# Performance work log

Measured on AMD Instinct MI355X. Metric: run time of the kernel, lower is better.

## Reference

```python
import jax, jax.numpy as jnp
import numpy as np

N, D_IN, UNITS = 8192, 2048, 2048


def setup_inputs() -> dict:
    key = jax.random.key(0)
    ks = jax.random.split(key, 14)
    s_in = 1.0 / np.sqrt(D_IN)
    s_u = 1.0 / np.sqrt(UNITS)
    return {
        "x": jax.random.normal(ks[0], (N, UNITS), jnp.float32),
        "y": jax.random.normal(ks[1], (N, D_IN), jnp.float32),
        # W* act on y (D_IN -> UNITS), U* act on x (UNITS -> UNITS)
        "Wz": jax.random.normal(ks[2], (D_IN, UNITS), jnp.float32) * s_in,
        "bz": jnp.zeros((UNITS,), jnp.float32),
        "Uz": jax.random.normal(ks[3], (UNITS, UNITS), jnp.float32) * s_u,
        "buz": jax.random.normal(ks[4], (UNITS,), jnp.float32) * 0.05,  # glorot-init bias
        "Wr": jax.random.normal(ks[5], (D_IN, UNITS), jnp.float32) * s_in,
        "br": jnp.zeros((UNITS,), jnp.float32),
        "Ur": jax.random.normal(ks[6], (UNITS, UNITS), jnp.float32) * s_u,
        "bur": jnp.zeros((UNITS,), jnp.float32),
        "Wg": jax.random.normal(ks[7], (D_IN, UNITS), jnp.float32) * s_in,
        "bg": jax.random.normal(ks[8], (UNITS,), jnp.float32) * 0.05,  # glorot-init bias
        "Ug": jax.random.normal(ks[9], (UNITS, UNITS), jnp.float32) * s_u,
        "bug": jnp.zeros((UNITS,), jnp.float32),
    }


def reference(x, y, Wz, bz, Uz, buz, Wr, br, Ur, bur, Wg, bg, Ug, bug):
    # Batch the three y-projections and the two x-projections into single GEMMs.
    Wy = y @ jnp.concatenate([Wz, Wr, Wg], axis=1)          # [N, 3*UNITS]
    Ux = x @ jnp.concatenate([Uz, Ur], axis=1)               # [N, 2*UNITS]
    u = Wz.shape[1]
    z = Wy[:, :u] + bz + Ux[:, :u] + buz                     # NOTE: no sigmoid (faithful to source)
    r = Wy[:, u:2 * u] + br + Ux[:, u:] + bur                # NOTE: no sigmoid (faithful to source)
    h = jnp.tanh(Wy[:, 2 * u:] + bg + (r * x) @ Ug + bug)
    return (1.0 - z) * x + z * h
```

## Files before the change

kernel.cpp:

```cpp
#include <hip/hip_runtime.h>
#include <hip/hip_bf16.h>
#include <cstdint>
#include <cmath>

typedef __bf16 bf16;
typedef __bf16 bf16x8 __attribute__((ext_vector_type(8)));
typedef __bf16 bf16x4 __attribute__((ext_vector_type(4)));
typedef float f32x4 __attribute__((ext_vector_type(4)));

#define NROWS 8192
#define UNITS 2048
#define NT 64
#define NSPLIT 32

__device__ __forceinline__ void gload_lds16(const bf16* g, const bf16* lds) {
  __builtin_amdgcn_global_load_lds(
      (const __attribute__((address_space(1))) uint32_t*)(uintptr_t)g,
      (__attribute__((address_space(3))) uint32_t*)(uint32_t)(uintptr_t)lds,
      16, 0, 0);
}

#define BARR do { asm volatile("" ::: "memory"); __builtin_amdgcn_s_barrier(); \
                  asm volatile("" ::: "memory"); } while (0)
#define WAITV4 asm volatile("s_waitcnt vmcnt(4)" ::: "memory")
#define LGKM8  asm volatile("s_waitcnt lgkmcnt(8)" ::: "memory")
#define LGKM0  asm volatile("s_waitcnt lgkmcnt(0)" ::: "memory")

__global__ void pack_xy_kernel(const float* __restrict__ x, const float* __restrict__ y,
                               bf16* __restrict__ xb, bf16* __restrict__ yb) {
  size_t n4 = (size_t)NROWS * UNITS / 4;
  size_t stride = (size_t)gridDim.x * blockDim.x;
  for (size_t i = (size_t)blockIdx.x * blockDim.x + threadIdx.x; i < n4; i += stride) {
    float4 vx = ((const float4*)x)[i];
    float4 vy = ((const float4*)y)[i];
    bf16x4 ox = {(bf16)vx.x, (bf16)vx.y, (bf16)vx.z, (bf16)vx.w};
    bf16x4 oy = {(bf16)vy.x, (bf16)vy.y, (bf16)vy.z, (bf16)vy.w};
    ((bf16x4*)xb)[i] = ox;
    ((bf16x4*)yb)[i] = oy;
  }
}

__global__ void transpose_cvt6_kernel(const float* __restrict__ Wz, const float* __restrict__ Uz,
                                      const float* __restrict__ Wr, const float* __restrict__ Ur,
                                      const float* __restrict__ Wg, const float* __restrict__ Ug,
                                      bf16* __restrict__ Bzr, bf16* __restrict__ Bgt) {
  __shared__ float t[32][33];
  const float* src;
  bf16* dst;
  int koff;
  switch (blockIdx.z) {
    case 0: src = Wz; dst = Bzr;                         koff = 0;    break;
    case 1: src = Uz; dst = Bzr;                         koff = 2048; break;
    case 2: src = Wr; dst = Bzr + (size_t)2048 * 4096;   koff = 0;    break;
    case 3: src = Ur; dst = Bzr + (size_t)2048 * 4096;   koff = 2048; break;
    case 4: src = Wg; dst = Bgt;                         koff = 0;    break;
    default: src = Ug; dst = Bgt;                        koff = 2048; break;
  }
  int j0 = blockIdx.x * 32, k0 = blockIdx.y * 32;
  int tx = threadIdx.x & 31, ty = threadIdx.x >> 5;
#pragma unroll
  for (int i = 0; i < 32; i += 8)
    t[ty + i][tx] = src[(size_t)(k0 + ty + i) * UNITS + j0 + tx];
  __syncthreads();
#pragma unroll
  for (int i = 0; i < 32; i += 8)
    dst[(size_t)(j0 + ty + i) * 4096 + koff + k0 + tx] = (bf16)t[tx][ty + i];
}

template <int EPI>
__global__ __launch_bounds__(512, 2)
void gemm256(const bf16* __restrict__ A0, const bf16* __restrict__ A1,
             const bf16* __restrict__ Bt,
             const float* __restrict__ bias_a, const float* __restrict__ bias_b,
             const float* __restrict__ bias_c, const float* __restrict__ bias_d,
             const float* __restrict__ xin, bf16* __restrict__ zbuf,
             bf16* __restrict__ rxbuf, float* __restrict__ outbuf) {
  __shared__ bf16 LDS[2][32768];
  const int tid = threadIdx.x;
  const int wv = tid >> 6, lane = tid & 63;
  const int wr = wv >> 2, wc = wv & 3;

  const int nl = (int)gridDim.x >> 3;
  const int xc = (int)blockIdx.x & 7;
  const int l = (int)blockIdx.x >> 3;
  const int bxq = nl >> 4;
  const int by = (xc & 1) * 16 + (l & 15);
  const int bx = (xc >> 1) * bxq + (l >> 4);
  const int brow = by * 256;
  const int bcol = bx * 256;

  const int rr = lane >> 2;
  const int kk_st = ((lane & 3) * 8) ^ ((rr & 6) << 2);
  int offA[2][2], offB[2][2], dstA[2][2], dstB[2][2];
#pragma unroll
  for (int H = 0; H < 2; ++H)
#pragma unroll
    for (int c = 0; c < 2; ++c) {
      int ssA = H * 8 + wv;
      offA[H][c] = (brow + c * 128 + (ssA >> 1) * 16 + rr) * 2048 + (ssA & 1) * 32 + kk_st;
      dstA[H][c] = c * 8192 + ssA * 512;
      int ssB = (wv >> 2) * 8 + H * 4 + (wv & 3);
      offB[H][c] = (bcol + c * 128 + (ssB >> 1) * 16 + rr) * 4096 + (ssB & 1) * 32 + kk_st;
      dstB[H][c] = 16384 + c * 8192 + ssB * 512;
    }

  const int lr = lane & 15;
  const int kread = ((lane >> 4) * 8) ^ ((lr & 6) << 2);
  const int abase = wr * 8192 + lr * 32 + kread;
  const int bbase = 16384 + (wc >> 1) * 8192 + (wc & 1) * 4096 + lr * 32 + kread;

#define ST_A(TI, H, BUF)                                                      \
  if ((TI) < NT) {                                                            \
    const bf16* _s = ((TI) < NSPLIT) ? A0 + (size_t)(TI)*64                   \
                                     : A1 + (size_t)((TI)-NSPLIT) * 64;       \
    gload_lds16(_s + offA[H][0], (BUF) + dstA[H][0]);                         \
    gload_lds16(_s + offA[H][1], (BUF) + dstA[H][1]);                         \
  }
#define ST_B(TI, H, BUF)                                                      \
  if ((TI) < NT) {                                                            \
    const bf16* _s = Bt + (size_t)(TI)*64;                                    \
    gload_lds16(_s + offB[H][0], (BUF) + dstB[H][0]);                         \
    gload_lds16(_s + offB[H][1], (BUF) + dstB[H][1]);                         \
  }
#define RD_B(DST, LP, NB)                                                     \
  _Pragma("unroll") for (int n = 0; n < 2; ++n)                               \
  _Pragma("unroll") for (int kh = 0; kh < 2; ++kh)                            \
      DST[n][kh] = *(const bf16x8*)((LP) + bbase + ((n + 2 * (NB)) * 2 + kh) * 512);
#define RD_A(DST, LP, MB)                                                     \
  _Pragma("unroll") for (int m = 0; m < 4; ++m)                               \
  _Pragma("unroll") for (int kh = 0; kh < 2; ++kh)                            \
      DST[m][kh] = *(const bf16x8*)((LP) + abase + ((m + 4 * (MB)) * 2 + kh) * 512);
#define MFMA_Q(AARR, BARR_, MOFF, NOFF)                                       \
  __builtin_amdgcn_s_setprio(1);                                              \
  _Pragma("unroll") for (int kh = 0; kh < 2; ++kh)                            \
  _Pragma("unroll") for (int m = 0; m < 4; ++m)                               \
  _Pragma("unroll") for (int n = 0; n < 2; ++n)                               \
      acc[m + MOFF][n + NOFF] = __builtin_amdgcn_mfma_f32_16x16x32_bf16(      \
          AARR[m][kh], BARR_[n][kh], acc[m + MOFF][n + NOFF], 0, 0, 0);       \
  __builtin_amdgcn_s_setprio(0);

  f32x4 acc[8][4];
#pragma unroll
  for (int m = 0; m < 8; ++m)
#pragma unroll
    for (int n = 0; n < 4; ++n) {
      f32x4 zz = {0.f, 0.f, 0.f, 0.f};
      acc[m][n] = zz;
    }

  {
    bf16* L0 = &LDS[0][0];
    bf16* L1 = &LDS[1][0];
    ST_B(0, 0, L0); ST_A(0, 0, L0);
    ST_A(0, 1, L0); ST_B(0, 1, L0);
    ST_B(1, 0, L1); ST_A(1, 0, L1);
    WAITV4;
    BARR;
  }

#define TILE(T, CUR, NXT)                                                     \
  {                                                                           \
    const bf16* Lc = &LDS[CUR][0];                                            \
    bf16* Lcw = &LDS[CUR][0];                                                 \
    bf16* Ln = &LDS[NXT][0];                                                  \
    bf16x8 a0[4][2], a1[4][2], b0[2][2], b1[2][2];                            \
                   \
    RD_A(a0, Lc, 0);                                                          \
    RD_B(b0, Lc, 0);                                                          \
    ST_A((T) + 1, 1, Ln);                                                     \
    LGKM8; BARR; LGKM0;                                                       \
    MFMA_Q(a0, b0, 0, 0);                                                     \
    BARR;                                                                     \
                       \
    RD_A(a1, Lc, 1);                                                          \
    ST_B((T) + 1, 1, Ln);                                                     \
    BARR; LGKM0;                                                              \
    MFMA_Q(a1, b0, 4, 0);                                                     \
    BARR;                                                                     \
                       \
    RD_B(b1, Lc, 1);                                                          \
    ST_B((T) + 2, 0, Lcw);                                                    \
    BARR; LGKM0;                                                              \
    MFMA_Q(a0, b1, 0, 2);                                                     \
    BARR;                                                                     \
                     \
    ST_A((T) + 2, 0, Lcw);                                                    \
    BARR;                                                                     \
    MFMA_Q(a1, b1, 4, 2);                                                     \
    WAITV4;                                                                   \
    BARR;                                                                     \
  }

#pragma unroll 1
  for (int t = 0; t < NT; t += 2) {
    TILE(t, 0, 1);
    TILE(t + 1, 1, 0);
  }

  const int lq = (lane >> 4) << 2;
  const int lc = lane & 15;
  const int rowb = brow + wr * 128;
  const int colb = bcol + wc * 64;
  if constexpr (EPI == 0) {
    if (bcol < UNITS) {
#pragma unroll
      for (int m = 0; m < 8; ++m)
#pragma unroll
        for (int n = 0; n < 4; ++n) {
          int col = colb + n * 16 + lc;
          float ba = bias_a[col] + bias_b[col];
#pragma unroll
          for (int q = 0; q < 4; ++q) {
            int row = rowb + m * 16 + lq + q;
            zbuf[(size_t)row * UNITS + col] = (bf16)(acc[m][n][q] + ba);
          }
        }
    } else {
#pragma unroll
      for (int m = 0; m < 8; ++m)
#pragma unroll
        for (int n = 0; n < 4; ++n) {
          int col = colb - UNITS + n * 16 + lc;
          float bc = bias_c[col] + bias_d[col];
#pragma unroll
          for (int q = 0; q < 4; ++q) {
            int row = rowb + m * 16 + lq + q;
            size_t idx = (size_t)row * UNITS + col;
            float r = acc[m][n][q] + bc;
            rxbuf[idx] = (bf16)(r * xin[idx]);
          }
        }
    }
  } else {
#pragma unroll
    for (int m = 0; m < 8; ++m)
#pragma unroll
      for (int n = 0; n < 4; ++n) {
        int col = colb + n * 16 + lc;
        float bg_ = bias_a[col] + bias_b[col];
#pragma unroll
        for (int q = 0; q < 4; ++q) {
          int row = rowb + m * 16 + lq + q;
          size_t idx = (size_t)row * UNITS + col;
          float h = tanhf(acc[m][n][q] + bg_);
          float zv = (float)zbuf[idx];
          float xv = xin[idx];
          outbuf[idx] = (1.f - zv) * xv + zv * h;
        }
      }
  }
#undef ST_A
#undef ST_B
#undef RD_A
#undef RD_B
#undef MFMA_Q
#undef TILE
}

extern "C" void kernel_launch(void* const* d_in, const int* in_sizes, int n_in,
                              void* d_out, int out_size, void* d_ws, size_t ws_size,
                              hipStream_t stream) {
  const float* x   = (const float*)d_in[0];
  const float* y   = (const float*)d_in[1];
  const float* Wz  = (const float*)d_in[2];
  const float* bz  = (const float*)d_in[3];
  const float* Uz  = (const float*)d_in[4];
  const float* buz = (const float*)d_in[5];
  const float* Wr  = (const float*)d_in[6];
  const float* br  = (const float*)d_in[7];
  const float* Ur  = (const float*)d_in[8];
  const float* bur = (const float*)d_in[9];
  const float* Wg  = (const float*)d_in[10];
  const float* bg  = (const float*)d_in[11];
  const float* Ug  = (const float*)d_in[12];
  const float* bug = (const float*)d_in[13];
  float* out = (float*)d_out;

  char* w = (char*)d_ws;
  bf16* Ybf = (bf16*)w;  w += (size_t)NROWS * UNITS * 2;
  bf16* Xbf = (bf16*)w;  w += (size_t)NROWS * UNITS * 2;
  bf16* RX  = (bf16*)w;  w += (size_t)NROWS * UNITS * 2;
  bf16* Bzr = (bf16*)w;  w += (size_t)4096 * 4096 * 2;
  bf16* Bgt = (bf16*)w;  w += (size_t)2048 * 4096 * 2;
  bf16* Zb  = (bf16*)w;  w += (size_t)NROWS * UNITS * 2;

  pack_xy_kernel<<<2048, 256, 0, stream>>>(x, y, Xbf, Ybf);
  dim3 tg(64, 64, 6);
  transpose_cvt6_kernel<<<tg, 256, 0, stream>>>(Wz, Uz, Wr, Ur, Wg, Ug, Bzr, Bgt);

  gemm256<0><<<512, 512, 0, stream>>>(Ybf, Xbf, Bzr, bz, buz, br, bur, x, Zb, RX, nullptr);
  gemm256<1><<<256, 512, 0, stream>>>(Ybf, RX, Bgt, bg, bug, nullptr, nullptr, x, Zb, nullptr, out);
}
```

Baseline: 503.8 us.

## Restructure GEMM main loop to prefetch next tile's LDS fragments during MFMAs

Reorders the double-buffered GEMM inner loop so that global-to-LDS stores and LDS register reads for the next quarter or next tile are issued before each MFMA block. Fragment registers are hoisted out of the tile so the first fragments of tile t+1 are read during tile t. The separate lgkmcnt waits are removed, vmcnt waits are made per-stage with a peeled tail, and sched_barrier is added to pin the schedule. The aim is to hide LDS and global latency behind MFMA work, at the cost of more live registers and finer-grained wait accounting that must exactly match the number of issued loads.

```diff
diff --git a/kernel.cpp b/kernel.cpp
--- a/kernel.cpp
+++ b/kernel.cpp
@@ -21,10 +21,8 @@
 }
 
 #define BARR do { asm volatile("" ::: "memory"); __builtin_amdgcn_s_barrier(); \
-                  asm volatile("" ::: "memory"); } while (0)
-#define WAITV4 asm volatile("s_waitcnt vmcnt(4)" ::: "memory")
-#define LGKM8  asm volatile("s_waitcnt lgkmcnt(8)" ::: "memory")
-#define LGKM0  asm volatile("s_waitcnt lgkmcnt(0)" ::: "memory")
+                  __builtin_amdgcn_sched_barrier(0); asm volatile("" ::: "memory"); } while (0)
+#define WAITN(N) asm volatile("s_waitcnt vmcnt(" #N ")" ::: "memory")
 
 __global__ void pack_xy_kernel(const float* __restrict__ x, const float* __restrict__ y,
                                bf16* __restrict__ xb, bf16* __restrict__ yb) {
@@ -148,54 +146,54 @@
       acc[m][n] = zz;
     }
 
+  bf16x8 a0[4][2], a1[4][2], b0[2][2], b1[2][2];
+
   {
     bf16* L0 = &LDS[0][0];
     bf16* L1 = &LDS[1][0];
-    ST_B(0, 0, L0); ST_A(0, 0, L0);
-    ST_A(0, 1, L0); ST_B(0, 1, L0);
-    ST_B(1, 0, L1); ST_A(1, 0, L1);
-    WAITV4;
+    ST_A(0, 0, L0); ST_B(0, 0, L0); ST_B(0, 1, L0); ST_A(0, 1, L0);
+    ST_A(1, 0, L1); ST_B(1, 0, L1); ST_B(1, 1, L1);
+    WAITN(8);
     BARR;
-  }
-
-#define TILE(T, CUR, NXT)                                                     \
+    RD_A(a0, L0, 0);
+    RD_B(b0, L0, 0);
+  }
+
+#define TILE(T, CUR, NXT, W1, W2, W3, W4)                                     \
   {                                                                           \
     const bf16* Lc = &LDS[CUR][0];                                            \
     bf16* Lcw = &LDS[CUR][0];                                                 \
-    bf16* Ln = &LDS[NXT][0];                                                  \
-    bf16x8 a0[4][2], a1[4][2], b0[2][2], b1[2][2];                            \
-                   \
-    RD_A(a0, Lc, 0);                                                          \
-    RD_B(b0, Lc, 0);                                                          \
-    ST_A((T) + 1, 1, Ln);                                                     \
-    LGKM8; BARR; LGKM0;                                                       \
+    const bf16* Ln = &LDS[NXT][0];                                            \
+    bf16* Lnw = &LDS[NXT][0];                                                 \
+                                                                      \
+    ST_A((T) + 1, 1, Lnw);                                                    \
+    RD_B(b1, Lc, 1);                                                          \
     MFMA_Q(a0, b0, 0, 0);                                                     \
-    BARR;                                                                     \
-                       \
+    WAITN(W1); BARR;                                                          \
+                                                                      \
+    ST_A((T) + 2, 0, Lcw);                                                    \
     RD_A(a1, Lc, 1);                                                          \
-    ST_B((T) + 1, 1, Ln);                                                     \
-    BARR; LGKM0;                                                              \
+    MFMA_Q(a0, b1, 0, 2);                                                     \
+    WAITN(W2); BARR;                                                          \
+                                                                      \
+    ST_B((T) + 2, 0, Lcw);                                                    \
+    if ((T) + 1 < NT) { RD_A(a0, Ln, 0); }                                    \
     MFMA_Q(a1, b0, 4, 0);                                                     \
-    BARR;                                                                     \
-                       \
-    RD_B(b1, Lc, 1);                                                          \
-    ST_B((T) + 2, 0, Lcw);                                                    \
-    BARR; LGKM0;                                                              \
-    MFMA_Q(a0, b1, 0, 2);                                                     \
-    BARR;                                                                     \
-                     \
-    ST_A((T) + 2, 0, Lcw);                                                    \
-    BARR;                                                                     \
+    WAITN(W3); BARR;                                                          \
+                                                                      \
+    ST_B((T) + 2, 1, Lcw);                                                    \
+    if ((T) + 1 < NT) { RD_B(b0, Ln, 0); }                                    \
     MFMA_Q(a1, b1, 4, 2);                                                     \
-    WAITV4;                                                                   \
-    BARR;                                                                     \
+    WAITN(W4); BARR;                                                          \
   }
 
 #pragma unroll 1
-  for (int t = 0; t < NT; t += 2) {
-    TILE(t, 0, 1);
-    TILE(t + 1, 1, 0);
-  }
+  for (int t = 0; t < NT - 2; t += 2) {
+    TILE(t, 0, 1, 8, 8, 8, 8);
+    TILE(t + 1, 1, 0, 8, 8, 8, 8);
+  }
+  TILE(NT - 2, 0, 1, 8, 6, 4, 2);
+  TILE(NT - 1, 1, 0, 0, 0, 0, 0);
 
   const int lq = (lane >> 4) << 2;
   const int lc = lane & 15;
```

After: 700.9 us. +39.1%, slower.
